# Kernel tuning notes

Measured on AMD Instinct MI355X. Metric: run time of the kernel, lower is better.

## Reference

```python
import jax, jax.numpy as jnp
import numpy as np


def _rho_index(H, W, numangle, numrho):
    # Faithful to deep-hough-transform CUDA initTab + forward kernel:
    #   irho = int(sqrt(H^2+W^2)+1) / (numrho-1); theta_a = a*pi/numangle
    #   r = round((x - W//2)*cos/irho + (y - H//2)*sin/irho) + numrho//2
    irho = int(np.sqrt(H * H + W * W) + 1) / float(numrho - 1)
    itheta = np.pi / numangle
    ang = np.arange(numangle) * itheta
    tab_cos = (np.cos(ang) / irho).astype(np.float32)
    tab_sin = (np.sin(ang) / irho).astype(np.float32)
    x = (np.arange(W) - W // 2).astype(np.float32)
    y = (np.arange(H) - H // 2).astype(np.float32)
    # r[a, y, x]: rho bin each pixel votes into, per angle
    r = np.round(x[None, None, :] * tab_cos[:, None, None]
                 + y[None, :, None] * tab_sin[:, None, None]).astype(np.int32)
    r += numrho // 2
    r = np.clip(r, 0, numrho - 1)  # kernel assumes in-range; clip for safety
    return jnp.asarray(r.reshape(numangle, H * W))


def setup_inputs() -> dict:
    key = jax.random.key(0)
    N, C, H, W = 8, 128, 128, 128
    feat = jax.random.normal(key, (N, C, H, W), dtype=jnp.float32)
    return {"feat": feat, "numangle": 120, "numrho": 120}


def reference(feat, numangle, numrho):
    N, C, H, W = feat.shape
    idx = _rho_index(H, W, numangle, numrho)          # (A, H*W) int32, static
    f = feat.reshape(N * C, H * W).T                  # (H*W, N*C)
    # For each angle, scatter-add all pixel values into their rho bin.
    per_angle = lambda ia: jax.ops.segment_sum(f, ia, num_segments=numrho)  # (R, N*C)
    out = jax.vmap(per_angle)(idx)                    # (A, R, N*C)
    return out.transpose(2, 0, 1).reshape(N, C, numangle, numrho)
```

## Files before the change

### kernel.cpp

```cpp
#include <hip/hip_runtime.h>
#include <hip/hip_bf16.h>

#define NC    1024
#define HW    16384
#define HH    128
#define WW    128
#define NA    120
#define NR    120
#define PI_D  3.14159265358979323846

#define WS_FEATT   0UL
#define WS_OUTT    67108864UL
#define WS_PLIST   (67108864UL + 58982400UL)
#define WS_TABS    (126091264UL + 3932160UL)
#define WS_CNTS    (130023424UL + 1024UL)
#define WS_OFFS    (130024448UL + 57600UL + 64UL)

__global__ void k_tab(float* __restrict__ tabs) {
    int a = threadIdx.x;
    if (a < NA) {
        double itheta = PI_D / (double)NA;
        double diag   = sqrt((double)(HH * HH + WW * WW));
        double irho   = floor(diag + 1.0) / (double)(NR - 1);
        double ang    = (double)a * itheta;
        tabs[a]       = (float)(cos(ang) / irho);
        tabs[NA + a]  = (float)(sin(ang) / irho);
    }
}

__device__ __forceinline__ int rho_bin(int p, float tc, float ts) {
#pragma clang fp contract(off)
    int y = p >> 7, x = p & (WW - 1);
    float u = (float)(x - WW / 2) * tc;
    float v = (float)(y - HH / 2) * ts;
    float s = u + v;
    int r = (int)rintf(s) + NR / 2;
    return min(NR - 1, max(0, r));
}

__global__ __launch_bounds__(256) void k_count(const float* __restrict__ tabs,
                                               int* __restrict__ cnts) {
    __shared__ int cnt[NR];
    int a = blockIdx.x, t = threadIdx.x;
    if (t < NR) cnt[t] = 0;
    __syncthreads();
    float tc = tabs[a], ts = tabs[NA + a];
    for (int p = t; p < HW; p += 256)
        atomicAdd(&cnt[rho_bin(p, tc, ts)], 1);
    __syncthreads();
    if (t < NR) cnts[a * NR + t] = cnt[t];
}

__global__ void k_scan(const int* __restrict__ cnts, int* __restrict__ offs) {
    int a = threadIdx.x;
    if (a < NA) {
        int base = 0;
        for (int r = 0; r < NR; ++r) {
            offs[a * (NR + 1) + r] = base;
            base += cnts[a * NR + r];
        }
        offs[a * (NR + 1) + NR] = base;
    }
}

__global__ __launch_bounds__(256) void k_scatter(const float* __restrict__ tabs,
                                                 const int* __restrict__ offs,
                                                 unsigned short* __restrict__ plist) {
    __shared__ int cur[NR];
    int a = blockIdx.x, t = threadIdx.x;
    if (t < NR) cur[t] = offs[a * (NR + 1) + t];
    __syncthreads();
    float tc = tabs[a], ts = tabs[NA + a];
    for (int p = t; p < HW; p += 256) {
        int r = rho_bin(p, tc, ts);
        int pos = atomicAdd(&cur[r], 1);
        plist[a * HW + pos] = (unsigned short)p;
    }
}

__global__ __launch_bounds__(256) void k_tr_in(const float* __restrict__ in,
                                               float* __restrict__ outp) {
    __shared__ float tile[32][33];
    int p0 = blockIdx.x * 32;
    int c0 = blockIdx.y * 32;
    int tx = threadIdx.x, ty = threadIdx.y;
    for (int i = 0; i < 32; i += 8)
        tile[ty + i][tx] = in[(size_t)(c0 + ty + i) * HW + p0 + tx];
    __syncthreads();
    for (int i = 0; i < 32; i += 8)
        outp[(size_t)(p0 + ty + i) * NC + c0 + tx] = tile[tx][ty + i];
}

__global__ __launch_bounds__(256) void k_gather(const float4* __restrict__ featT4,
                                                const int* __restrict__ offs,
                                                const unsigned short* __restrict__ plist,
                                                float4* __restrict__ outT4) {
    const int r = blockIdx.x;
    const int a = blockIdx.y;
    const int t = threadIdx.x;
    const unsigned short* pl = plist + (size_t)a * HW;

    const int k0 = offs[a * (NR + 1) + r];
    const int k1 = offs[a * (NR + 1) + r + 1];

    float4 a0 = {0.f, 0.f, 0.f, 0.f}, a1 = a0, a2 = a0, a3 = a0;
    int k = k0;
    for (; k + 8 <= k1; k += 8) {
        int p0 = pl[k + 0], p1 = pl[k + 1], p2 = pl[k + 2], p3 = pl[k + 3];
        int p4 = pl[k + 4], p5 = pl[k + 5], p6 = pl[k + 6], p7 = pl[k + 7];
        float4 v0 = featT4[(size_t)p0 * 256 + t];
        float4 v1 = featT4[(size_t)p1 * 256 + t];
        float4 v2 = featT4[(size_t)p2 * 256 + t];
        float4 v3 = featT4[(size_t)p3 * 256 + t];
        float4 v4 = featT4[(size_t)p4 * 256 + t];
        float4 v5 = featT4[(size_t)p5 * 256 + t];
        float4 v6 = featT4[(size_t)p6 * 256 + t];
        float4 v7 = featT4[(size_t)p7 * 256 + t];
        a0.x += v0.x; a0.y += v0.y; a0.z += v0.z; a0.w += v0.w;
        a1.x += v1.x; a1.y += v1.y; a1.z += v1.z; a1.w += v1.w;
        a2.x += v2.x; a2.y += v2.y; a2.z += v2.z; a2.w += v2.w;
        a3.x += v3.x; a3.y += v3.y; a3.z += v3.z; a3.w += v3.w;
        a0.x += v4.x; a0.y += v4.y; a0.z += v4.z; a0.w += v4.w;
        a1.x += v5.x; a1.y += v5.y; a1.z += v5.z; a1.w += v5.w;
        a2.x += v6.x; a2.y += v6.y; a2.z += v6.z; a2.w += v6.w;
        a3.x += v7.x; a3.y += v7.y; a3.z += v7.z; a3.w += v7.w;
    }
    for (; k + 4 <= k1; k += 4) {
        int p0 = pl[k + 0], p1 = pl[k + 1], p2 = pl[k + 2], p3 = pl[k + 3];
        float4 v0 = featT4[(size_t)p0 * 256 + t];
        float4 v1 = featT4[(size_t)p1 * 256 + t];
        float4 v2 = featT4[(size_t)p2 * 256 + t];
        float4 v3 = featT4[(size_t)p3 * 256 + t];
        a0.x += v0.x; a0.y += v0.y; a0.z += v0.z; a0.w += v0.w;
        a1.x += v1.x; a1.y += v1.y; a1.z += v1.z; a1.w += v1.w;
        a2.x += v2.x; a2.y += v2.y; a2.z += v2.z; a2.w += v2.w;
        a3.x += v3.x; a3.y += v3.y; a3.z += v3.z; a3.w += v3.w;
    }
    for (; k < k1; ++k) {
        float4 v = featT4[(size_t)pl[k] * 256 + t];
        a0.x += v.x; a0.y += v.y; a0.z += v.z; a0.w += v.w;
    }
    float4 s;
    s.x = (a0.x + a1.x) + (a2.x + a3.x);
    s.y = (a0.y + a1.y) + (a2.y + a3.y);
    s.z = (a0.z + a1.z) + (a2.z + a3.z);
    s.w = (a0.w + a1.w) + (a2.w + a3.w);
    outT4[(size_t)(a * NR + r) * 256 + t] = s;
}

__global__ __launch_bounds__(256) void k_tr_out(const float* __restrict__ in,
                                                float* __restrict__ outp) {
    __shared__ float tile[32][33];
    int j0 = blockIdx.x * 32;
    int c0 = blockIdx.y * 32;
    int tx = threadIdx.x, ty = threadIdx.y;
    for (int i = 0; i < 32; i += 8)
        tile[ty + i][tx] = in[(size_t)(j0 + ty + i) * NC + c0 + tx];
    __syncthreads();
    for (int i = 0; i < 32; i += 8)
        outp[(size_t)(c0 + ty + i) * (NA * NR) + j0 + tx] = tile[tx][ty + i];
}

extern "C" void kernel_launch(void* const* d_in, const int* in_sizes, int n_in,
                              void* d_out, int out_size, void* d_ws, size_t ws_size,
                              hipStream_t stream) {
    (void)in_sizes; (void)n_in; (void)out_size; (void)ws_size;
    const float* feat = (const float*)d_in[0];
    float* out = (float*)d_out;
    char* ws = (char*)d_ws;

    float*          featT = (float*)(ws + WS_FEATT);
    float*          outT  = (float*)(ws + WS_OUTT);
    unsigned short* plist = (unsigned short*)(ws + WS_PLIST);
    float*          tabs  = (float*)(ws + WS_TABS);
    int*            cnts  = (int*)(ws + WS_CNTS);
    int*            offs  = (int*)(ws + WS_OFFS);

    k_tab    <<<1, 128, 0, stream>>>(tabs);
    k_count  <<<NA, 256, 0, stream>>>(tabs, cnts);
    k_scan   <<<1, 128, 0, stream>>>(cnts, offs);
    k_scatter<<<NA, 256, 0, stream>>>(tabs, offs, plist);
    k_tr_in  <<<dim3(HW / 32, NC / 32), dim3(32, 8), 0, stream>>>(feat, featT);
    k_gather <<<dim3(NR, NA), 256, 0, stream>>>(
        (const float4*)featT, offs, plist, (float4*)outT);
    k_tr_out <<<dim3((NA * NR) / 32, NC / 32), dim3(32, 8), 0, stream>>>(outT, out);
}
```

Baseline: 1.111 ms.

## Split gather by pixel-row groups for L2 locality, then reduce partials

Result: no change. 1.115 ms (+0.4%).

```diff
diff --git a/kernel.cpp b/kernel.cpp
--- a/kernel.cpp
+++ b/kernel.cpp
@@ -7,14 +7,29 @@
 #define WW    128
 #define NA    120
 #define NR    120
+#define G     8
+#define NB2   (G * NR)
 #define PI_D  3.14159265358979323846
 
-#define WS_FEATT   0UL
-#define WS_OUTT    67108864UL
-#define WS_PLIST   (67108864UL + 58982400UL)
-#define WS_TABS    (126091264UL + 3932160UL)
-#define WS_CNTS    (130023424UL + 1024UL)
-#define WS_OFFS    (130024448UL + 57600UL + 64UL)
+typedef float vfloat4 __attribute__((ext_vector_type(4)));
+
+#define WS_FEATT 0UL
+#define WS_PLIST 67108864UL
+#define WS_OFFS2 71041024UL
+#define WS_CNTS2 71503872UL
+#define WS_TABS  71964672UL
+#define WS_RB    71965696UL
+#define WS_BASE  71969792UL
+#define WS_PART  72351744UL
+#define PART_CAP 80000UL
+#define WS_NEEDED (WS_PART + PART_CAP * 4096UL)
+
+#define F_FEATT 0UL
+#define F_OUTT  67108864UL
+#define F_PLIST (67108864UL + 58982400UL)
+#define F_TABS  (126091264UL + 3932160UL)
+#define F_CNTS  (130023424UL + 1024UL)
+#define F_OFFS  (130024448UL + 57600UL + 64UL)
 
 __global__ void k_tab(float* __restrict__ tabs) {
     int a = threadIdx.x;
@@ -38,6 +53,191 @@
     return min(NR - 1, max(0, r));
 }
 
+__device__ __forceinline__ int key2(int p, float tc, float ts) {
+    return (p >> 11) * NR + rho_bin(p, tc, ts);
+}
+
+__device__ __forceinline__ float4 accum_bin(const float4* __restrict__ f4,
+                                            const unsigned short* __restrict__ pl,
+                                            int k0, int k1, int t) {
+    float4 a0 = {0.f, 0.f, 0.f, 0.f}, a1 = a0, a2 = a0, a3 = a0;
+    int k = k0;
+    for (; k + 8 <= k1; k += 8) {
+        int p0 = pl[k + 0], p1 = pl[k + 1], p2 = pl[k + 2], p3 = pl[k + 3];
+        int p4 = pl[k + 4], p5 = pl[k + 5], p6 = pl[k + 6], p7 = pl[k + 7];
+        float4 v0 = f4[(size_t)p0 * 256 + t];
+        float4 v1 = f4[(size_t)p1 * 256 + t];
+        float4 v2 = f4[(size_t)p2 * 256 + t];
+        float4 v3 = f4[(size_t)p3 * 256 + t];
+        float4 v4 = f4[(size_t)p4 * 256 + t];
+        float4 v5 = f4[(size_t)p5 * 256 + t];
+        float4 v6 = f4[(size_t)p6 * 256 + t];
+        float4 v7 = f4[(size_t)p7 * 256 + t];
+        a0.x += v0.x; a0.y += v0.y; a0.z += v0.z; a0.w += v0.w;
+        a1.x += v1.x; a1.y += v1.y; a1.z += v1.z; a1.w += v1.w;
+        a2.x += v2.x; a2.y += v2.y; a2.z += v2.z; a2.w += v2.w;
+        a3.x += v3.x; a3.y += v3.y; a3.z += v3.z; a3.w += v3.w;
+        a0.x += v4.x; a0.y += v4.y; a0.z += v4.z; a0.w += v4.w;
+        a1.x += v5.x; a1.y += v5.y; a1.z += v5.z; a1.w += v5.w;
+        a2.x += v6.x; a2.y += v6.y; a2.z += v6.z; a2.w += v6.w;
+        a3.x += v7.x; a3.y += v7.y; a3.z += v7.z; a3.w += v7.w;
+    }
+    for (; k + 4 <= k1; k += 4) {
+        int p0 = pl[k + 0], p1 = pl[k + 1], p2 = pl[k + 2], p3 = pl[k + 3];
+        float4 v0 = f4[(size_t)p0 * 256 + t];
+        float4 v1 = f4[(size_t)p1 * 256 + t];
+        float4 v2 = f4[(size_t)p2 * 256 + t];
+        float4 v3 = f4[(size_t)p3 * 256 + t];
+        a0.x += v0.x; a0.y += v0.y; a0.z += v0.z; a0.w += v0.w;
+        a1.x += v1.x; a1.y += v1.y; a1.z += v1.z; a1.w += v1.w;
+        a2.x += v2.x; a2.y += v2.y; a2.z += v2.z; a2.w += v2.w;
+        a3.x += v3.x; a3.y += v3.y; a3.z += v3.z; a3.w += v3.w;
+    }
+    for (; k < k1; ++k) {
+        float4 v = f4[(size_t)pl[k] * 256 + t];
+        a0.x += v.x; a0.y += v.y; a0.z += v.z; a0.w += v.w;
+    }
+    float4 s;
+    s.x = (a0.x + a1.x) + (a2.x + a3.x);
+    s.y = (a0.y + a1.y) + (a2.y + a3.y);
+    s.z = (a0.z + a1.z) + (a2.z + a3.z);
+    s.w = (a0.w + a1.w) + (a2.w + a3.w);
+    return s;
+}
+
+
+__global__ __launch_bounds__(256) void k_count2(const float* __restrict__ tabs,
+                                                int* __restrict__ cnts2) {
+    __shared__ int cnt[NB2];
+    int a = blockIdx.x, t = threadIdx.x;
+    for (int i = t; i < NB2; i += 256) cnt[i] = 0;
+    __syncthreads();
+    float tc = tabs[a], ts = tabs[NA + a];
+    for (int p = t; p < HW; p += 256)
+        atomicAdd(&cnt[key2(p, tc, ts)], 1);
+    __syncthreads();
+    for (int i = t; i < NB2; i += 256) cnts2[a * NB2 + i] = cnt[i];
+}
+
+__global__ void k_scan2(const int* __restrict__ cnts2, int* __restrict__ offs2) {
+    int a = threadIdx.x;
+    if (a < NA) {
+        int base = 0;
+        for (int b = 0; b < NB2; ++b) {
+            offs2[a * (NB2 + 1) + b] = base;
+            base += cnts2[a * NB2 + b];
+        }
+        offs2[a * (NB2 + 1) + NB2] = base;
+    }
+}
+
+__global__ __launch_bounds__(256) void k_scatter2(const float* __restrict__ tabs,
+                                                  const int* __restrict__ offs2,
+                                                  unsigned short* __restrict__ plist) {
+    __shared__ int cur[NB2];
+    int a = blockIdx.x, t = threadIdx.x;
+    for (int i = t; i < NB2; i += 256) cur[i] = offs2[a * (NB2 + 1) + i];
+    __syncthreads();
+    float tc = tabs[a], ts = tabs[NA + a];
+    for (int p = t; p < HW; p += 256) {
+        int pos = atomicAdd(&cur[key2(p, tc, ts)], 1);
+        plist[(size_t)a * HW + pos] = (unsigned short)p;
+    }
+}
+
+__global__ void k_meta(const int* __restrict__ offs2, int* __restrict__ rb,
+                       int* __restrict__ basep) {
+    __shared__ int aw[NA], ab[NA];
+    int t = threadIdx.x;
+    int w[G], rmn[G];
+    if (t < NA) {
+        int tot = 0;
+#pragma unroll
+        for (int g = 0; g < G; ++g) {
+            const int* po = offs2 + t * (NB2 + 1) + g * NR;
+            int rmin = NR, rmax = -1;
+            for (int r = 0; r < NR; ++r)
+                if (po[r + 1] > po[r]) { if (r < rmin) rmin = r; rmax = r; }
+            rmn[g] = rmin;
+            w[g]   = rmax - rmin + 1;
+            tot += w[g];
+        }
+        aw[t] = tot;
+#pragma unroll
+        for (int g = 0; g < G; ++g) rb[t * G + g] = rmn[g];
+    }
+    __syncthreads();
+    if (t == 0) {
+        int run = 0;
+        for (int i = 0; i < NA; ++i) { ab[i] = run; run += aw[i]; }
+    }
+    __syncthreads();
+    if (t < NA) {
+        int b = ab[t];
+#pragma unroll
+        for (int g = 0; g < G; ++g) { basep[t * G + g] = b; b += w[g]; }
+    }
+}
+
+__global__ __launch_bounds__(256) void k_tr_in(const float* __restrict__ in,
+                                               float* __restrict__ outp) {
+    __shared__ float tile[32][33];
+    int p0 = blockIdx.x * 32, c0 = blockIdx.y * 32;
+    int tx = threadIdx.x, ty = threadIdx.y;
+    for (int i = 0; i < 32; i += 8)
+        tile[ty + i][tx] = in[(size_t)(c0 + ty + i) * HW + p0 + tx];
+    __syncthreads();
+    for (int i = 0; i < 32; i += 8)
+        outp[(size_t)(p0 + ty + i) * NC + c0 + tx] = tile[tx][ty + i];
+}
+
+__global__ __launch_bounds__(256) void k_gather2(const float4* __restrict__ featT4,
+        const int* __restrict__ offs2, const unsigned short* __restrict__ plist,
+        const int* __restrict__ rb, const int* __restrict__ basep,
+        vfloat4* __restrict__ part4) {
+    const int g = blockIdx.x, a = blockIdx.y, s = blockIdx.z;
+    const int t = threadIdx.x;
+    const unsigned short* pl = plist + (size_t)a * HW;
+    const int* po = offs2 + a * (NB2 + 1) + g * NR;
+    const long mb = (long)basep[a * G + g] - rb[a * G + g];
+    for (int r = s; r < NR; r += 2) {
+        int k0 = po[r], k1 = po[r + 1];
+        if (k0 == k1) continue;
+        float4 v = accum_bin(featT4, pl, k0, k1, t);
+        vfloat4 w = {v.x, v.y, v.z, v.w};
+        __builtin_nontemporal_store(w, &part4[(size_t)(mb + r) * 256 + t]);
+    }
+}
+
+__global__ __launch_bounds__(256) void k_reduce(const float4* __restrict__ part4,
+        const int* __restrict__ offs2, const int* __restrict__ rb,
+        const int* __restrict__ basep, float4* __restrict__ outT4) {
+    const int r = blockIdx.x, a = blockIdx.y, t = threadIdx.x;
+    float4 s = {0.f, 0.f, 0.f, 0.f};
+#pragma unroll
+    for (int g = 0; g < G; ++g) {
+        int b = a * (NB2 + 1) + g * NR + r;
+        if (offs2[b + 1] > offs2[b]) {
+            float4 v = part4[(size_t)(basep[a * G + g] + r - rb[a * G + g]) * 256 + t];
+            s.x += v.x; s.y += v.y; s.z += v.z; s.w += v.w;
+        }
+    }
+    outT4[(size_t)(a * NR + r) * 256 + t] = s;
+}
+
+__global__ __launch_bounds__(256) void k_tr_out(const float* __restrict__ in,
+                                                float* __restrict__ outp) {
+    __shared__ float tile[32][33];
+    int j0 = blockIdx.x * 32, c0 = blockIdx.y * 32;
+    int tx = threadIdx.x, ty = threadIdx.y;
+    for (int i = 0; i < 32; i += 8)
+        tile[ty + i][tx] = in[(size_t)(j0 + ty + i) * NC + c0 + tx];
+    __syncthreads();
+    for (int i = 0; i < 32; i += 8)
+        outp[(size_t)(c0 + ty + i) * (NA * NR) + j0 + tx] = tile[tx][ty + i];
+}
+
+
 __global__ __launch_bounds__(256) void k_count(const float* __restrict__ tabs,
                                                int* __restrict__ cnts) {
     __shared__ int cnt[NR];
@@ -74,114 +274,68 @@
     for (int p = t; p < HW; p += 256) {
         int r = rho_bin(p, tc, ts);
         int pos = atomicAdd(&cur[r], 1);
-        plist[a * HW + pos] = (unsigned short)p;
-    }
-}
-
-__global__ __launch_bounds__(256) void k_tr_in(const float* __restrict__ in,
-                                               float* __restrict__ outp) {
-    __shared__ float tile[32][33];
-    int p0 = blockIdx.x * 32;
-    int c0 = blockIdx.y * 32;
-    int tx = threadIdx.x, ty = threadIdx.y;
-    for (int i = 0; i < 32; i += 8)
-        tile[ty + i][tx] = in[(size_t)(c0 + ty + i) * HW + p0 + tx];
-    __syncthreads();
-    for (int i = 0; i < 32; i += 8)
-        outp[(size_t)(p0 + ty + i) * NC + c0 + tx] = tile[tx][ty + i];
+        plist[(size_t)a * HW + pos] = (unsigned short)p;
+    }
 }
 
 __global__ __launch_bounds__(256) void k_gather(const float4* __restrict__ featT4,
                                                 const int* __restrict__ offs,
                                                 const unsigned short* __restrict__ plist,
                                                 float4* __restrict__ outT4) {
-    const int r = blockIdx.x;
-    const int a = blockIdx.y;
-    const int t = threadIdx.x;
+    const int r = blockIdx.x, a = blockIdx.y, t = threadIdx.x;
     const unsigned short* pl = plist + (size_t)a * HW;
-
-    const int k0 = offs[a * (NR + 1) + r];
-    const int k1 = offs[a * (NR + 1) + r + 1];
-
-    float4 a0 = {0.f, 0.f, 0.f, 0.f}, a1 = a0, a2 = a0, a3 = a0;
-    int k = k0;
-    for (; k + 8 <= k1; k += 8) {
-        int p0 = pl[k + 0], p1 = pl[k + 1], p2 = pl[k + 2], p3 = pl[k + 3];
-        int p4 = pl[k + 4], p5 = pl[k + 5], p6 = pl[k + 6], p7 = pl[k + 7];
-        float4 v0 = featT4[(size_t)p0 * 256 + t];
-        float4 v1 = featT4[(size_t)p1 * 256 + t];
-        float4 v2 = featT4[(size_t)p2 * 256 + t];
-        float4 v3 = featT4[(size_t)p3 * 256 + t];
-        float4 v4 = featT4[(size_t)p4 * 256 + t];
-        float4 v5 = featT4[(size_t)p5 * 256 + t];
-        float4 v6 = featT4[(size_t)p6 * 256 + t];
-        float4 v7 = featT4[(size_t)p7 * 256 + t];
-        a0.x += v0.x; a0.y += v0.y; a0.z += v0.z; a0.w += v0.w;
-        a1.x += v1.x; a1.y += v1.y; a1.z += v1.z; a1.w += v1.w;
-        a2.x += v2.x; a2.y += v2.y; a2.z += v2.z; a2.w += v2.w;
-        a3.x += v3.x; a3.y += v3.y; a3.z += v3.z; a3.w += v3.w;
-        a0.x += v4.x; a0.y += v4.y; a0.z += v4.z; a0.w += v4.w;
-        a1.x += v5.x; a1.y += v5.y; a1.z += v5.z; a1.w += v5.w;
-        a2.x += v6.x; a2.y += v6.y; a2.z += v6.z; a2.w += v6.w;
-        a3.x += v7.x; a3.y += v7.y; a3.z += v7.z; a3.w += v7.w;
-    }
-    for (; k + 4 <= k1; k += 4) {
-        int p0 = pl[k + 0], p1 = pl[k + 1], p2 = pl[k + 2], p3 = pl[k + 3];
-        float4 v0 = featT4[(size_t)p0 * 256 + t];
-        float4 v1 = featT4[(size_t)p1 * 256 + t];
-        float4 v2 = featT4[(size_t)p2 * 256 + t];
-        float4 v3 = featT4[(size_t)p3 * 256 + t];
-        a0.x += v0.x; a0.y += v0.y; a0.z += v0.z; a0.w += v0.w;
-        a1.x += v1.x; a1.y += v1.y; a1.z += v1.z; a1.w += v1.w;
-        a2.x += v2.x; a2.y += v2.y; a2.z += v2.z; a2.w += v2.w;
-        a3.x += v3.x; a3.y += v3.y; a3.z += v3.z; a3.w += v3.w;
-    }
-    for (; k < k1; ++k) {
-        float4 v = featT4[(size_t)pl[k] * 256 + t];
-        a0.x += v.x; a0.y += v.y; a0.z += v.z; a0.w += v.w;
-    }
-    float4 s;
-    s.x = (a0.x + a1.x) + (a2.x + a3.x);
-    s.y = (a0.y + a1.y) + (a2.y + a3.y);
-    s.z = (a0.z + a1.z) + (a2.z + a3.z);
-    s.w = (a0.w + a1.w) + (a2.w + a3.w);
+    int k0 = offs[a * (NR + 1) + r];
+    int k1 = offs[a * (NR + 1) + r + 1];
+    float4 s = accum_bin(featT4, pl, k0, k1, t);
     outT4[(size_t)(a * NR + r) * 256 + t] = s;
 }
 
-__global__ __launch_bounds__(256) void k_tr_out(const float* __restrict__ in,
-                                                float* __restrict__ outp) {
-    __shared__ float tile[32][33];
-    int j0 = blockIdx.x * 32;
-    int c0 = blockIdx.y * 32;
-    int tx = threadIdx.x, ty = threadIdx.y;
-    for (int i = 0; i < 32; i += 8)
-        tile[ty + i][tx] = in[(size_t)(j0 + ty + i) * NC + c0 + tx];
-    __syncthreads();
-    for (int i = 0; i < 32; i += 8)
-        outp[(size_t)(c0 + ty + i) * (NA * NR) + j0 + tx] = tile[tx][ty + i];
-}
 
 extern "C" void kernel_launch(void* const* d_in, const int* in_sizes, int n_in,
                               void* d_out, int out_size, void* d_ws, size_t ws_size,
                               hipStream_t stream) {
-    (void)in_sizes; (void)n_in; (void)out_size; (void)ws_size;
+    (void)in_sizes; (void)n_in; (void)out_size;
     const float* feat = (const float*)d_in[0];
     float* out = (float*)d_out;
     char* ws = (char*)d_ws;
 
-    float*          featT = (float*)(ws + WS_FEATT);
-    float*          outT  = (float*)(ws + WS_OUTT);
-    unsigned short* plist = (unsigned short*)(ws + WS_PLIST);
-    float*          tabs  = (float*)(ws + WS_TABS);
-    int*            cnts  = (int*)(ws + WS_CNTS);
-    int*            offs  = (int*)(ws + WS_OFFS);
-
-    k_tab    <<<1, 128, 0, stream>>>(tabs);
-    k_count  <<<NA, 256, 0, stream>>>(tabs, cnts);
-    k_scan   <<<1, 128, 0, stream>>>(cnts, offs);
-    k_scatter<<<NA, 256, 0, stream>>>(tabs, offs, plist);
-    k_tr_in  <<<dim3(HW / 32, NC / 32), dim3(32, 8), 0, stream>>>(feat, featT);
-    k_gather <<<dim3(NR, NA), 256, 0, stream>>>(
-        (const float4*)featT, offs, plist, (float4*)outT);
-    k_tr_out <<<dim3((NA * NR) / 32, NC / 32), dim3(32, 8), 0, stream>>>(outT, out);
-}
+    if (ws_size >= WS_NEEDED) {
+        float*          featT = (float*)(ws + WS_FEATT);
+        float*          outT  = (float*)(ws + WS_FEATT);
+        unsigned short* plist = (unsigned short*)(ws + WS_PLIST);
+        int*            offs2 = (int*)(ws + WS_OFFS2);
+        int*            cnts2 = (int*)(ws + WS_CNTS2);
+        float*          tabs  = (float*)(ws + WS_TABS);
+        int*            rb    = (int*)(ws + WS_RB);
+        int*            basep = (int*)(ws + WS_BASE);
+        float*          part  = (float*)(ws + WS_PART);
+
+        k_tab     <<<1, 128, 0, stream>>>(tabs);
+        k_count2  <<<NA, 256, 0, stream>>>(tabs, cnts2);
+        k_scan2   <<<1, 128, 0, stream>>>(cnts2, offs2);
+        k_scatter2<<<NA, 256, 0, stream>>>(tabs, offs2, plist);
+        k_meta    <<<1, 128, 0, stream>>>(offs2, rb, basep);
+        k_tr_in   <<<dim3(HW / 32, NC / 32), dim3(32, 8), 0, stream>>>(feat, featT);
+        k_gather2 <<<dim3(G, NA, 2), 256, 0, stream>>>(
+            (const float4*)featT, offs2, plist, rb, basep, (vfloat4*)part);
+        k_reduce  <<<dim3(NR, NA), 256, 0, stream>>>(
+            (const float4*)part, offs2, rb, basep, (float4*)outT);
+        k_tr_out  <<<dim3((NA * NR) / 32, NC / 32), dim3(32, 8), 0, stream>>>(outT, out);
+    } else {
+        float*          featT = (float*)(ws + F_FEATT);
+        float*          outT  = (float*)(ws + F_OUTT);
+        unsigned short* plist = (unsigned short*)(ws + F_PLIST);
+        float*          tabs  = (float*)(ws + F_TABS);
+        int*            cnts  = (int*)(ws + F_CNTS);
+        int*            offs  = (int*)(ws + F_OFFS);
+
+        k_tab    <<<1, 128, 0, stream>>>(tabs);
+        k_count  <<<NA, 256, 0, stream>>>(tabs, cnts);
+        k_scan   <<<1, 128, 0, stream>>>(cnts, offs);
+        k_scatter<<<NA, 256, 0, stream>>>(tabs, offs, plist);
+        k_tr_in  <<<dim3(HW / 32, NC / 32), dim3(32, 8), 0, stream>>>(feat, featT);
+        k_gather <<<dim3(NR, NA), 256, 0, stream>>>(
+            (const float4*)featT, offs, plist, (float4*)outT);
+        k_tr_out <<<dim3((NA * NR) / 32, NC / 32), dim3(32, 8), 0, stream>>>(outT, out);
+    }
+}
```
